# Kernel optimization log

Measured on AMD Instinct MI355X. Metric: run time of the kernel, lower is better.

The kernel has to match this reference:

```python
import jax, jax.numpy as jnp
import numpy as np

B = 8192
BASE = 340            # base_state_size (one frame)
STACK = 4             # frame stack -> state_size = 1360
SLOT_F = 4            # [present, dx, dy, dist] per slot
CAT_DEFS = [16, 8, 4, 4, 4, 8, 8, 8, 8]   # slots per category (sum = 68)
NUM_CATS = len(CAT_DEFS)
CAT_INFO = []
_off = 59
for _slots in CAT_DEFS:
    CAT_INFO.append((_off, _slots))
    _off += 1 + _slots * SLOT_F
STATE_SIZE = BASE * STACK
ATTN_DIM, HEADS = 128, 4
HEAD_DIM = ATTN_DIM // HEADS
TRUNK_H = 1024
ATOMS = 51
ACTIONS = 81
TRUNK_IN = STATE_SIZE + ATTN_DIM
NEG_INF = -1e9


def _layernorm(x, g, b, eps=1e-5):
    m = x.mean(-1, keepdims=True)
    v = ((x - m) ** 2).mean(-1, keepdims=True)
    return (x - m) * jax.lax.rsqrt(v + eps) * g + b


def setup_inputs() -> dict:
    key = jax.random.key(0)
    ks = iter(jax.random.split(key, 32))
    def w(shape, s=0.02):
        return jax.random.normal(next(ks), shape, jnp.float32) * s
    return {
        "state": jax.random.normal(next(ks), (B, STATE_SIZE), jnp.float32),
        "embed_W": w((7, ATTN_DIM)), "embed_b": jnp.zeros((ATTN_DIM,), jnp.float32),
        "ln_g": jnp.ones((ATTN_DIM,), jnp.float32), "ln_b": jnp.zeros((ATTN_DIM,), jnp.float32),
        "cls_tok": jnp.zeros((1, 1, ATTN_DIM), jnp.float32),
        "in_proj_W": w((3 * ATTN_DIM, ATTN_DIM)), "in_proj_b": jnp.zeros((3 * ATTN_DIM,), jnp.float32),
        "out_proj_W": w((ATTN_DIM, ATTN_DIM)), "out_proj_b": jnp.zeros((ATTN_DIM,), jnp.float32),
        "t0_W": w((TRUNK_IN, TRUNK_H)), "t0_b": jnp.zeros((TRUNK_H,), jnp.float32),
        "t0_g": jnp.ones((TRUNK_H,), jnp.float32), "t0_beta": jnp.zeros((TRUNK_H,), jnp.float32),
        "t1_W": w((TRUNK_H, TRUNK_H)), "t1_b": jnp.zeros((TRUNK_H,), jnp.float32),
        "t1_g": jnp.ones((TRUNK_H,), jnp.float32), "t1_beta": jnp.zeros((TRUNK_H,), jnp.float32),
        "val_fc_W": w((TRUNK_H, TRUNK_H // 2)), "val_fc_b": jnp.zeros((TRUNK_H // 2,), jnp.float32),
        "val_out_W": w((TRUNK_H // 2, ATOMS)), "val_out_b": jnp.zeros((ATOMS,), jnp.float32),
        "adv_fc_W": w((TRUNK_H, TRUNK_H // 2)), "adv_fc_b": jnp.zeros((TRUNK_H // 2,), jnp.float32),
        "adv_out_W": w((TRUNK_H // 2, ACTIONS * ATOMS)), "adv_out_b": jnp.zeros((ACTIONS * ATOMS,), jnp.float32),
    }


def _build_tokens(state):
    """Per-category gather + delta + pack -> (B, 68, 7) tokens and (B, 68) empty-mask."""
    b = state.shape[0]
    latest_off = (STACK - 1) * BASE
    prev_off = (STACK - 2) * BASE
    toks, masks = [], []
    for cat_id, (base, slots) in enumerate(CAT_INFO):
        lo = latest_off + base + 1
        po = prev_off + base + 1
        latest = state[:, lo:lo + slots * SLOT_F].reshape(b, slots, SLOT_F)
        prev = state[:, po:po + slots * SLOT_F].reshape(b, slots, SLOT_F)
        present = latest[:, :, 0]
        dx, dy, dist = latest[:, :, 1:2], latest[:, :, 2:3], latest[:, :, 3:4]
        vel_valid = ((present > 0.5) & (prev[:, :, 0] > 0.5))[:, :, None].astype(state.dtype)
        ddx = (dx - prev[:, :, 1:2]) * vel_valid
        ddy = (dy - prev[:, :, 2:3]) * vel_valid
        cat_norm = jnp.full((b, slots, 1), cat_id / (NUM_CATS - 1), state.dtype)
        toks.append(jnp.concatenate([dx, dy, dist, ddx, ddy, cat_norm, present[:, :, None]], axis=2))
        masks.append(present < 0.5)
    tokens = jnp.concatenate(toks, axis=1)
    mask = jnp.concatenate(masks, axis=1)          # True = slot empty
    all_empty = jnp.all(mask, axis=1, keepdims=True)
    mask = mask & ~all_empty                       # if everything empty, unmask all
    return tokens, mask


def reference(state, embed_W, embed_b, ln_g, ln_b, cls_tok, in_proj_W, in_proj_b,
              out_proj_W, out_proj_b, t0_W, t0_b, t0_g, t0_beta, t1_W, t1_b, t1_g, t1_beta,
              val_fc_W, val_fc_b, val_out_W, val_out_b, adv_fc_W, adv_fc_b, adv_out_W, adv_out_b):
    b = state.shape[0]
    tokens, mask = _build_tokens(state)
    x = _layernorm(tokens @ embed_W + embed_b, ln_g, ln_b)
    x = jnp.concatenate([jnp.broadcast_to(cls_tok, (b, 1, ATTN_DIM)), x], axis=1)  # (B, S+1, E)
    kpm = jnp.concatenate([jnp.zeros((b, 1), bool), mask], axis=1)                  # (B, S+1)
    qkv = x @ in_proj_W.T + in_proj_b
    q, k, v = jnp.split(qkv, 3, axis=-1)
    def to_heads(t):
        return t.reshape(b, -1, HEADS, HEAD_DIM).transpose(0, 2, 1, 3)
    q, k, v = to_heads(q), to_heads(k), to_heads(v)
    scores = jnp.einsum('bhqd,bhkd->bhqk', q, k) / np.float32(np.sqrt(HEAD_DIM))
    scores = jnp.where(kpm[:, None, None, :], NEG_INF, scores)
    attn = jax.nn.softmax(scores, axis=-1)
    out = jnp.einsum('bhqk,bhkd->bhqd', attn, v).transpose(0, 2, 1, 3).reshape(b, -1, ATTN_DIM)
    out = out @ out_proj_W.T + out_proj_b
    pooled = out[:, 0, :]                           # CLS pooling
    h = jnp.concatenate([state, pooled], axis=1)
    h = jax.nn.relu(_layernorm(h @ t0_W + t0_b, t0_g, t0_beta))
    h = jax.nn.relu(_layernorm(h @ t1_W + t1_b, t1_g, t1_beta))
    val = jax.nn.relu(h @ val_fc_W + val_fc_b)
    val = (val @ val_out_W + val_out_b).reshape(b, 1, ATOMS)
    adv = jax.nn.relu(h @ adv_fc_W + adv_fc_b)
    adv = (adv @ adv_out_W + adv_out_b).reshape(b, ACTIONS, ATOMS)
    q_atoms = val + adv - adv.mean(axis=1, keepdims=True)
    return jax.nn.softmax(q_atoms, axis=2)          # (B, 81, 51) C51 probabilities
```

## Files before the change

kernel.cpp:

```cpp
#include <hip/hip_runtime.h>

typedef unsigned short u16;
typedef unsigned int u32;
typedef __attribute__((ext_vector_type(4))) unsigned int u32x4;
typedef __attribute__((ext_vector_type(8))) __bf16 bf16x8;
typedef __attribute__((ext_vector_type(4))) float f32x4;

#define MFMA(a, b, c) __builtin_amdgcn_mfma_f32_16x16x32_bf16(a, b, c, 0, 0, 0)

__device__ __forceinline__ float b2f(u16 h) {
    union { unsigned int u; float f; } v; v.u = ((unsigned int)h) << 16; return v.f;
}
__device__ __forceinline__ u16 f2b(float f) {
    union { float f; unsigned int u; } v; v.f = f;
    unsigned int r = v.u + 0x7fffu + ((v.u >> 16) & 1u);
    return (u16)(r >> 16);
}
__device__ __forceinline__ float gread(const void* p, size_t i, int isf32) {
    return isf32 ? ((const float*)p)[i] : b2f(((const u16*)p)[i]);
}
__device__ __forceinline__ void gl_lds16(const u16* g, u16* l) {
    __builtin_amdgcn_global_load_lds(
        (const __attribute__((address_space(1))) void*)(g),
        (__attribute__((address_space(3))) void*)(l), 16, 0, 0);
}

__global__ __launch_bounds__(256) void detect_kernel(const void* __restrict__ state,
                                                     int* __restrict__ flag)
{
    __shared__ int cnt;
    if (threadIdx.x == 0) cnt = 0;
    __syncthreads();
    const u16* p = (const u16*)state;
    int local = 0;
    for (int i = threadIdx.x; i < 4096; i += 256) {
        int e = (p[i] >> 7) & 0xFF;
        if (e >= 200) local++;
    }
    atomicAdd(&cnt, local);
    __syncthreads();
    if (threadIdx.x == 0) *flag = (cnt >= 32) ? 1 : 0;
}

__global__ __launch_bounds__(256) void norm_small_kernel(
    const void* __restrict__ embW, const void* __restrict__ embB,
    const void* __restrict__ lng,  const void* __restrict__ lnb,
    const void* __restrict__ cls,  const void* __restrict__ ipW,
    const void* __restrict__ ipb,  const void* __restrict__ opW,
    const void* __restrict__ opb,  const void* __restrict__ t0g,
    const void* __restrict__ t0be, const void* __restrict__ t1g,
    const void* __restrict__ t1be, u16* __restrict__ dst,
    const int* __restrict__ flagp)
{
    int idx = blockIdx.x * 256 + threadIdx.x;
    if (idx >= 71552) return;
    int isf32 = *flagp;
    const void* src; int rel;
    if      (idx < 896)   { src = embW; rel = idx; }
    else if (idx < 1024)  { src = embB; rel = idx - 896; }
    else if (idx < 1152)  { src = lng;  rel = idx - 1024; }
    else if (idx < 1280)  { src = lnb;  rel = idx - 1152; }
    else if (idx < 1408)  { src = cls;  rel = idx - 1280; }
    else if (idx < 50560) { src = ipW;  rel = idx - 1408; }
    else if (idx < 50944) { src = ipb;  rel = idx - 50560; }
    else if (idx < 67328) { src = opW;  rel = idx - 50944; }
    else if (idx < 67456) { src = opb;  rel = idx - 67328; }
    else if (idx < 68480) { src = t0g;  rel = idx - 67456; }
    else if (idx < 69504) { src = t0be; rel = idx - 68480; }
    else if (idx < 70528) { src = t1g;  rel = idx - 69504; }
    else                  { src = t1be; rel = idx - 70528; }
    dst[idx] = isf32 ? f2b(((const float*)src)[rel]) : ((const u16*)src)[rel];
}

__global__ __launch_bounds__(256) void pack_kernel(
    const void* __restrict__ t0W, const void* __restrict__ t1W,
    const void* __restrict__ vfW, const void* __restrict__ afW,
    const void* __restrict__ voW, const void* __restrict__ aoW,
    const void* __restrict__ t0b, const void* __restrict__ t1b,
    const void* __restrict__ vfb, const void* __restrict__ afb,
    const void* __restrict__ vob, const void* __restrict__ aob,
    const int* __restrict__ flagp,
    u16* __restrict__ Bt0, u16* __restrict__ Bt1, u16* __restrict__ Btfc,
    u16* __restrict__ Btao,
    float* __restrict__ bias0, float* __restrict__ bias1, float* __restrict__ biasfc,
    float* __restrict__ biasao)
{
    int idx = blockIdx.x * 256 + threadIdx.x;
    const int isf32 = *flagp;
    if (idx < 1540096) {
        int n = idx / 1504, k = idx % 1504;
        Bt0[idx] = (k < 1488) ? f2b(gread(t0W, (size_t)k * 1024 + n, isf32)) : (u16)0;
        return;
    }
    idx -= 1540096;
    if (idx < 1048576) {
        int n = idx >> 10, k = idx & 1023;
        Bt1[idx] = f2b(gread(t1W, (size_t)k * 1024 + n, isf32));
        return;
    }
    idx -= 1048576;
    if (idx < 1048576) {
        int n = idx >> 10, k = idx & 1023;
        Btfc[idx] = (n < 512) ? f2b(gread(vfW, (size_t)k * 512 + n, isf32))
                              : f2b(gread(afW, (size_t)k * 512 + (n - 512), isf32));
        return;
    }
    idx -= 1048576;
    if (idx < 2228224) {
        int n = idx / 512, k = idx & 511;
        u16 v = 0;
        if (n < 4131)                  v = f2b(gread(aoW, (size_t)k * 4131 + n, isf32));
        else if (n >= 4224 && n < 4275) v = f2b(gread(voW, (size_t)k * 51 + (n - 4224), isf32));
        Btao[idx] = v;
        return;
    }
    idx -= 2228224;
    if (idx < 1024) { bias0[idx] = gread(t0b, idx, isf32); return; }
    idx -= 1024;
    if (idx < 1024) { bias1[idx] = gread(t1b, idx, isf32); return; }
    idx -= 1024;
    if (idx < 1024) { biasfc[idx] = (idx < 512) ? gread(vfb, idx, isf32)
                                                : gread(afb, idx - 512, isf32); return; }
    idx -= 1024;
    if (idx < 4352) {
        float v = 0.f;
        if (idx < 4131) v = gread(aob, idx, isf32);
        else if (idx >= 4224 && idx < 4275) v = gread(vob, idx - 4224, isf32);
        biasao[idx] = v;
        return;
    }
}

__global__ __launch_bounds__(384) void prep_cls_kernel(
    const u16* __restrict__ cls, const u16* __restrict__ ipW, const u16* __restrict__ ipb,
    float* __restrict__ qvec, float* __restrict__ vcls, float* __restrict__ s0)
{
    __shared__ float qkv[384];
    int tid = threadIdx.x;
    float a = b2f(ipb[tid]);
    for (int c = 0; c < 128; c++) a += b2f(ipW[(size_t)tid * 128 + c]) * b2f(cls[c]);
    qkv[tid] = a;
    __syncthreads();
    if (tid < 128) { qvec[tid] = qkv[tid]; vcls[tid] = qkv[256 + tid]; }
    if (tid < 4) {
        float s = 0.f;
        for (int d = 0; d < 32; d++) s += qkv[tid * 32 + d] * qkv[128 + tid * 32 + d];
        s0[tid] = s * 0.17677669529663687f;
    }
}

__global__ __launch_bounds__(256) void prep2_kernel(
    const u16* __restrict__ ipW, const u16* __restrict__ ipb,
    const float* __restrict__ qvec, float* __restrict__ rmat, float* __restrict__ cb)
{
    int tid = threadIdx.x;
    for (int j = 0; j < 2; j++) {
        int idx = j * 256 + tid;
        int h = idx >> 7, c = idx & 127;
        float acc = 0.f;
        for (int k = 0; k < 32; k++)
            acc += qvec[32 * h + k] * b2f(ipW[(size_t)(128 + 32 * h + k) * 128 + c]);
        rmat[idx] = acc;
    }
    if (tid < 4) {
        float acc = 0.f;
        for (int k = 0; k < 32; k++)
            acc += qvec[32 * tid + k] * b2f(ipb[128 + 32 * tid + k]);
        cb[tid] = acc;
    }
}

__global__ __launch_bounds__(256) void attn_kernel(
    const void* __restrict__ state, const int* __restrict__ flagp,
    const u16* __restrict__ embW, const u16* __restrict__ embB,
    const u16* __restrict__ lng, const u16* __restrict__ lnb,
    const u16* __restrict__ ipW, const u16* __restrict__ ipb,
    const u16* __restrict__ opW, const u16* __restrict__ opb,
    const float* __restrict__ vcls, const float* __restrict__ s0,
    const float* __restrict__ rmat, const float* __restrict__ cb,
    u16* __restrict__ A0)
{
    __shared__ __align__(16) u16 Xs[68][138];
    __shared__ __align__(16) float rstk[4][33][4];
    __shared__ __align__(16) float embWs[896];
    __shared__ __align__(16) float tok[68][8];
    __shared__ __align__(16) float sc[68][4];
    __shared__ __align__(16) float pp[72][4];
    __shared__ __align__(16) float zs[4][128];
    __shared__ __align__(16) float yv[128];
    __shared__ u16 embBh[128], lngh[128], lnbh[128];
    __shared__ float maskf[68];
    __shared__ float cbs[4];
    __shared__ int   cnt;

    const int b   = blockIdx.x;
    const int tid = threadIdx.x;
    const int wave = tid >> 6, lane = tid & 63;
    const int isf32 = *flagp;
    u16* arow = A0 + (size_t)b * 1504;
    float* rowf = (float*)&Xs[0][0];

    for (int i = tid; i < 896; i += 256) embWs[i] = b2f(embW[i]);
    if (tid < 128) { embBh[tid] = embB[tid]; lngh[tid] = lng[tid]; lnbh[tid] = lnb[tid]; }
    for (int i = tid; i < 512; i += 256) {
        int h = i >> 7, c = i & 127;
        rstk[c >> 5][c & 31][h] = rmat[i];
    }
    if (tid < 4) cbs[tid] = cb[tid];
    if (tid == 0) cnt = 0;

    if (isf32) {
        const f32x4* srowf = (const f32x4*)((const float*)state + (size_t)b * 1360);
        for (int i = tid; i < 170; i += 256) {
            f32x4 v0 = srowf[i * 2], v1 = srowf[i * 2 + 1];
            union { u16 h[8]; u32x4 v; } u;
            #pragma unroll
            for (int j = 0; j < 4; j++) { u.h[j] = f2b(v0[j]); u.h[4 + j] = f2b(v1[j]); }
            *(u32x4*)&arow[i * 8] = u.v;
            *(f32x4*)&rowf[i * 8] = v0;
            *(f32x4*)&rowf[i * 8 + 4] = v1;
        }
    } else {
        const u16* srow = (const u16*)state + (size_t)b * 1360;
        for (int i = tid; i < 170; i += 256) {
            u32x4 v = *(const u32x4*)&srow[i * 8];
            *(u32x4*)&arow[i * 8] = v;
            union { u32x4 v; u16 h[8]; } u; u.v = v;
            f32x4 f0, f1;
            #pragma unroll
            for (int j = 0; j < 4; j++) { f0[j] = b2f(u.h[j]); f1[j] = b2f(u.h[4 + j]); }
            *(f32x4*)&rowf[i * 8] = f0;
            *(f32x4*)&rowf[i * 8 + 4] = f1;
        }
    }
    if (tid < 16) arow[1488 + tid] = 0;
    __syncthreads();

    if (tid < 68) {
        const int cum[10]    = {0, 16, 24, 28, 32, 36, 44, 52, 60, 68};
        const int basetab[9] = {59, 124, 157, 174, 191, 208, 241, 274, 307};
        int t = tid, cat = 0;
        while (t >= cum[cat + 1]) cat++;
        int slot = t - cum[cat];
        int off  = basetab[cat] + 1 + slot * 4;
        float lp    = rowf[1020 + off + 0];
        float ldx   = rowf[1020 + off + 1];
        float ldy   = rowf[1020 + off + 2];
        float ldist = rowf[1020 + off + 3];
        float ppres = rowf[680 + off + 0];
        float pdx   = rowf[680 + off + 1];
        float pdy   = rowf[680 + off + 2];
        float vv = (lp > 0.5f && ppres > 0.5f) ? 1.f : 0.f;
        tok[t][0] = ldx; tok[t][1] = ldy; tok[t][2] = ldist;
        tok[t][3] = (ldx - pdx) * vv; tok[t][4] = (ldy - pdy) * vv;
        tok[t][5] = (float)cat * 0.125f; tok[t][6] = lp;
        int m = (lp < 0.5f) ? 1 : 0;
        maskf[t] = (float)m;
        if (m) atomicAdd(&cnt, 1);
    }
    __syncthreads();
    const bool all_empty = (cnt == 68);

    for (int t = wave; t < 68; t += 4) {
        float e0 = b2f(embBh[lane]), e1 = b2f(embBh[lane + 64]);
        #pragma unroll
        for (int f = 0; f < 7; f++) {
            float tv = tok[t][f];
            e0 += tv * embWs[f * 128 + lane];
            e1 += tv * embWs[f * 128 + lane + 64];
        }
        float s = e0 + e1;
        #pragma unroll
        for (int m = 1; m < 64; m <<= 1) s += __shfl_xor(s, m);
        float mean = s * (1.f / 128.f);
        float d0 = e0 - mean, d1 = e1 - mean;
        float v = d0 * d0 + d1 * d1;
        #pragma unroll
        for (int m = 1; m < 64; m <<= 1) v += __shfl_xor(v, m);
        float inv = rsqrtf(v * (1.f / 128.f) + 1e-5f);
        Xs[t][lane]      = f2b(d0 * inv * b2f(lngh[lane])      + b2f(lnbh[lane]));
        Xs[t][lane + 64] = f2b(d1 * inv * b2f(lngh[lane + 64]) + b2f(lnbh[lane + 64]));
    }
    __syncthreads();

    for (int it = 0; it < 2; it++) {
        int idx = it * 256 + tid;
        if (idx < 272) {
            int t = idx >> 2, ks = idx & 3;
            const u32* xrow = (const u32*)&Xs[t][0] + ks * 16;
            f32x4 a = {0.f, 0.f, 0.f, 0.f};
            #pragma unroll
            for (int c = 0; c < 16; c++) {
                u32 w = xrow[c];
                union { u32 u; float f; } lo, hi;
                lo.u = w << 16; hi.u = w & 0xffff0000u;
                f32x4 r0 = *(const f32x4*)&rstk[ks][2 * c][0];
                f32x4 r1 = *(const f32x4*)&rstk[ks][2 * c + 1][0];
                a += lo.f * r0 + hi.f * r1;
            }
            #pragma unroll
            for (int m = 1; m < 4; m <<= 1) {
                a[0] += __shfl_xor(a[0], m);
                a[1] += __shfl_xor(a[1], m);
                a[2] += __shfl_xor(a[2], m);
                a[3] += __shfl_xor(a[3], m);
            }
            float v = (ks == 0) ? a[0] : (ks == 1) ? a[1] : (ks == 2) ? a[2] : a[3];
            float sv = (cbs[ks] + v) * 0.17677669529663687f;
            if (maskf[t] > 0.5f && !all_empty) sv = -1e9f;
            sc[t][ks] = sv;
        }
    }
    __syncthreads();

    {
        int h = wave;
        float v0 = (lane == 0) ? s0[h] : sc[lane - 1][h];
        float v1 = (lane <= 4) ? sc[lane + 63][h] : -1e30f;
        float m = fmaxf(v0, v1);
        #pragma unroll
        for (int mm = 1; mm < 64; mm <<= 1) m = fmaxf(m, __shfl_xor(m, mm));
        float e0 = __expf(v0 - m);
        float e1 = (lane <= 4) ? __expf(v1 - m) : 0.f;
        float sum = e0 + e1;
        #pragma unroll
        for (int mm = 1; mm < 64; mm <<= 1) sum += __shfl_xor(sum, mm);
        float rinv = 1.f / sum;
        pp[lane][h] = e0 * rinv;
        if (lane <= 4) pp[lane + 64][h] = e1 * rinv;
    }
    __syncthreads();

    {
        int c = tid & 127, h0 = (tid >> 7) * 2;
        float acc0 = 0.f, acc1 = 0.f;
        #pragma unroll 4
        for (int t = 0; t < 68; t++) {
            float x = b2f(Xs[t][c]);
            float2 p = *(const float2*)&pp[t + 1][h0];
            acc0 += p.x * x; acc1 += p.y * x;
        }
        zs[h0][c] = acc0; zs[h0 + 1][c] = acc1;
    }
    __syncthreads();

    {
        int d = tid >> 1, half = tid & 1, h = d >> 5;
        float acc = 0.f;
        const u16* wrow = ipW + (size_t)(256 + d) * 128 + 64 * half;
        const float* zrow = &zs[h][64 * half];
        #pragma unroll
        for (int j = 0; j < 8; j++) {
            bf16x8 w = *(const bf16x8*)(wrow + j * 8);
            #pragma unroll
            for (int k = 0; k < 8; k++) acc += (float)w[k] * zrow[j * 8 + k];
        }
        float other = __shfl_xor(acc, 1);
        if (half == 0) {
            float p0 = pp[0][h];
            yv[d] = acc + other + p0 * vcls[d] + (1.f - p0) * b2f(ipb[256 + d]);
        }
    }
    __syncthreads();

    {
        int e = tid >> 1, half = tid & 1;
        float acc = 0.f;
        const u16* wrow = opW + (size_t)e * 128 + 64 * half;
        const float* yrow = &yv[64 * half];
        #pragma unroll
        for (int j = 0; j < 8; j++) {
            bf16x8 w = *(const bf16x8*)(wrow + j * 8);
            #pragma unroll
            for (int k = 0; k < 8; k++) acc += (float)w[k] * yrow[j * 8 + k];
        }
        float other = __shfl_xor(acc, 1);
        if (half == 0) arow[1360 + e] = f2b(acc + other + b2f(opb[e]));
    }
}

template <int EPI>
__global__ __launch_bounds__(256) void gemm_bt(
    const u16* __restrict__ A, int lda, const u16* __restrict__ Bt, int ldb,
    const float* __restrict__ bias, void* __restrict__ Cout, int ldc, int K)
{
    __shared__ __align__(16) u16 As[128 * 32];
    __shared__ __align__(16) u16 Bs[128 * 32];
    const int tid = threadIdx.x;
    const int row0 = blockIdx.y * 128, col0 = blockIdx.x * 128;
    const int wave = tid >> 6, lane = tid & 63;
    const int wm = wave >> 1, wn = wave & 1;
    const int lr = lane & 15, lq = lane >> 4;

    f32x4 acc[4][4] = {};

    for (int k0 = 0; k0 < K; k0 += 32) {
        __syncthreads();
        #pragma unroll
        for (int j = 0; j < 2; j++) {
            int ci = j * 256 + wave * 64 + lane;
            int r = ci >> 2, q = ci & 3;
            int lbase = (j * 256 + wave * 64) * 8;
            gl_lds16(A  + (size_t)(row0 + r) * lda + k0 + q * 8, &As[lbase]);
            gl_lds16(Bt + (size_t)(col0 + r) * ldb + k0 + q * 8, &Bs[lbase]);
        }
        __syncthreads();
        bf16x8 af[4], bf[4];
        #pragma unroll
        for (int i = 0; i < 4; i++) af[i] = *(const bf16x8*)&As[(wm * 64 + i * 16 + lr) * 32 + lq * 8];
        #pragma unroll
        for (int j = 0; j < 4; j++) bf[j] = *(const bf16x8*)&Bs[(wn * 64 + j * 16 + lr) * 32 + lq * 8];
        #pragma unroll
        for (int i = 0; i < 4; i++)
            #pragma unroll
            for (int j = 0; j < 4; j++)
                acc[i][j] = MFMA(af[i], bf[j], acc[i][j]);
    }

    const int cbase = col0 + wn * 64;
    const int rbase = row0 + wm * 64;
    float bv[4];
    #pragma unroll
    for (int j = 0; j < 4; j++) bv[j] = bias[cbase + j * 16 + lr];
    #pragma unroll
    for (int i = 0; i < 4; i++) {
        #pragma unroll
        for (int j = 0; j < 4; j++) {
            int cc = cbase + j * 16 + lr;
            #pragma unroll
            for (int r = 0; r < 4; r++) {
                int rr = rbase + i * 16 + lq * 4 + r;
                float v = acc[i][j][r] + bv[j];
                if (EPI == 1) v = fmaxf(v, 0.f);
                if (EPI == 0) ((float*)Cout)[(size_t)rr * ldc + cc] = v;
                else          ((u16*)Cout)[(size_t)rr * ldc + cc] = f2b(v);
            }
        }
    }
}

__global__ __launch_bounds__(256) void ln_relu_kernel(
    const float* __restrict__ C, const u16* __restrict__ g, const u16* __restrict__ be,
    u16* __restrict__ H)
{
    __shared__ float red[8];
    const int b = blockIdx.x, tid = threadIdx.x;
    const float* row = C + (size_t)b * 1024;
    float x0 = row[tid], x1 = row[tid + 256], x2 = row[tid + 512], x3 = row[tid + 768];
    float s = x0 + x1 + x2 + x3;
    #pragma unroll
    for (int m = 1; m < 64; m <<= 1) s += __shfl_xor(s, m);
    if ((tid & 63) == 0) red[tid >> 6] = s;
    __syncthreads();
    float mean = (red[0] + red[1] + red[2] + red[3]) * (1.f / 1024.f);
    float d0 = x0 - mean, d1 = x1 - mean, d2 = x2 - mean, d3 = x3 - mean;
    float v = d0 * d0 + d1 * d1 + d2 * d2 + d3 * d3;
    #pragma unroll
    for (int m = 1; m < 64; m <<= 1) v += __shfl_xor(v, m);
    if ((tid & 63) == 0) red[4 + (tid >> 6)] = v;
    __syncthreads();
    float inv = rsqrtf((red[4] + red[5] + red[6] + red[7]) * (1.f / 1024.f) + 1e-5f);
    u16* hrow = H + (size_t)b * 1024;
    float dd[4] = {d0, d1, d2, d3};
    #pragma unroll
    for (int i = 0; i < 4; i++) {
        int c = tid + i * 256;
        float h = dd[i] * inv * b2f(g[c]) + b2f(be[c]);
        hrow[c] = f2b(fmaxf(h, 0.f));
    }
}

__global__ __launch_bounds__(256) void final_kernel(
    const u16* __restrict__ ADV, void* __restrict__ out, const int* __restrict__ flagp)
{
    __shared__ __align__(16) u16 advr[4136];
    __shared__ float meanv[51];
    __shared__ float valv[51];
    const int b = blockIdx.x, tid = threadIdx.x;
    const int isf32 = *flagp;
    const u16* arow = ADV + (size_t)b * 4352;
    for (int i = tid; i < 517; i += 256)
        *(u32x4*)&advr[i * 8] = *(const u32x4*)&arow[i * 8];
    if (tid < 51) valv[tid] = b2f(arow[4224 + tid]);
    __syncthreads();
    if (tid < 51) {
        float s = 0.f;
        for (int j = 0; j < 81; j++) s += b2f(advr[j * 51 + tid]);
        meanv[tid] = s * (1.f / 81.f);
    }
    __syncthreads();
    const int wave = tid >> 6, lane = tid & 63;
    for (int a = wave; a < 81; a += 4) {
        float q = (lane < 51) ? valv[lane] + b2f(advr[a * 51 + lane]) - meanv[lane] : -1e30f;
        float m = q;
        #pragma unroll
        for (int mm = 1; mm < 64; mm <<= 1) m = fmaxf(m, __shfl_xor(m, mm));
        float e = (lane < 51) ? __expf(q - m) : 0.f;
        float s = e;
        #pragma unroll
        for (int mm = 1; mm < 64; mm <<= 1) s += __shfl_xor(s, mm);
        if (lane < 51) {
            float r = e / s;
            size_t oi = (size_t)b * 4131 + a * 51 + lane;
            if (isf32) ((float*)out)[oi] = r;
            else       ((u16*)out)[oi]  = f2b(r);
        }
    }
}

extern "C" void kernel_launch(void* const* d_in, const int* in_sizes, int n_in,
                              void* d_out, int out_size, void* d_ws, size_t ws_size,
                              hipStream_t stream)
{
    (void)in_sizes; (void)n_in; (void)out_size; (void)ws_size;
    const void* state = d_in[0];
    const void* embW  = d_in[1];
    const void* embB  = d_in[2];
    const void* lng   = d_in[3];
    const void* lnb   = d_in[4];
    const void* cls   = d_in[5];
    const void* ipW   = d_in[6];
    const void* ipb   = d_in[7];
    const void* opW   = d_in[8];
    const void* opb   = d_in[9];
    const void* t0W   = d_in[10];
    const void* t0b   = d_in[11];
    const void* t0g   = d_in[12];
    const void* t0be  = d_in[13];
    const void* t1W   = d_in[14];
    const void* t1b   = d_in[15];
    const void* t1g   = d_in[16];
    const void* t1be  = d_in[17];
    const void* vfW   = d_in[18];
    const void* vfb   = d_in[19];
    const void* voW   = d_in[20];
    const void* vob   = d_in[21];
    const void* afW   = d_in[22];
    const void* afb   = d_in[23];
    const void* aoW   = d_in[24];
    const void* aob   = d_in[25];

    char* ws = (char*)d_ws;
    size_t off = 0;
    auto alloc = [&](size_t bytes) -> void* {
        off = (off + 255) & ~(size_t)255;
        void* p = ws + off;
        off += bytes;
        return p;
    };
    int*   flag   = (int*)alloc(4);
    u16*   Nbuf   = (u16*)alloc(71552 * 2);
    float* qvec   = (float*)alloc(128 * 4);
    float* vcls   = (float*)alloc(128 * 4);
    float* s0     = (float*)alloc(4 * 4);
    float* rmat   = (float*)alloc(512 * 4);
    float* cb     = (float*)alloc(4 * 4);
    float* bias0  = (float*)alloc(1024 * 4);
    float* bias1  = (float*)alloc(1024 * 4);
    float* biasfc = (float*)alloc(1024 * 4);
    float* biasao = (float*)alloc(4352 * 4);
    u16* Bt0  = (u16*)alloc(1024L * 1504 * 2);
    u16* Bt1  = (u16*)alloc(1024L * 1024 * 2);
    u16* Btfc = (u16*)alloc(1024L * 1024 * 2);
    u16* Btao = (u16*)alloc(4352L * 512 * 2);
    u16* A0   = (u16*)alloc(8192L * 1504 * 2);
    float* C0 = (float*)alloc(8192L * 1024 * 4);
    u16* H0   = (u16*)alloc(8192L * 1024 * 2);
    u16* ADV  = A0;
    u16* H1   = (u16*)alloc(8192L * 1024 * 2);
    u16* VA   = (u16*)alloc(8192L * 1024 * 2);

    u16* Nemb  = Nbuf + 0;
    u16* NembB = Nbuf + 896;
    u16* Nlng  = Nbuf + 1024;
    u16* Nlnb  = Nbuf + 1152;
    u16* Ncls  = Nbuf + 1280;
    u16* Nipw  = Nbuf + 1408;
    u16* Nipb  = Nbuf + 50560;
    u16* Nopw  = Nbuf + 50944;
    u16* Nopb  = Nbuf + 67328;
    u16* Nt0g  = Nbuf + 67456;
    u16* Nt0be = Nbuf + 68480;
    u16* Nt1g  = Nbuf + 69504;
    u16* Nt1be = Nbuf + 70528;

    detect_kernel<<<1, 256, 0, stream>>>(state, flag);
    norm_small_kernel<<<280, 256, 0, stream>>>(embW, embB, lng, lnb, cls, ipW, ipb,
                                               opW, opb, t0g, t0be, t1g, t1be,
                                               Nbuf, flag);
    pack_kernel<<<22941, 256, 0, stream>>>(t0W, t1W, vfW, afW, voW, aoW,
                                           t0b, t1b, vfb, afb, vob, aob, flag,
                                           Bt0, Bt1, Btfc, Btao,
                                           bias0, bias1, biasfc, biasao);
    prep_cls_kernel<<<1, 384, 0, stream>>>(Ncls, Nipw, Nipb, qvec, vcls, s0);
    prep2_kernel<<<1, 256, 0, stream>>>(Nipw, Nipb, qvec, rmat, cb);
    attn_kernel<<<8192, 256, 0, stream>>>(state, flag, Nemb, NembB, Nlng, Nlnb,
                                          Nipw, Nipb, Nopw, Nopb,
                                          vcls, s0, rmat, cb, A0);
    gemm_bt<0><<<dim3(8, 64), 256, 0, stream>>>(A0, 1504, Bt0, 1504, bias0, C0, 1024, 1504);
    ln_relu_kernel<<<8192, 256, 0, stream>>>(C0, Nt0g, Nt0be, H0);
    gemm_bt<0><<<dim3(8, 64), 256, 0, stream>>>(H0, 1024, Bt1, 1024, bias1, C0, 1024, 1024);
    ln_relu_kernel<<<8192, 256, 0, stream>>>(C0, Nt1g, Nt1be, H1);
    gemm_bt<1><<<dim3(8, 64), 256, 0, stream>>>(H1, 1024, Btfc, 1024, biasfc, VA, 1024, 1024);
    gemm_bt<2><<<dim3(33, 64), 256, 0, stream>>>(VA + 512, 1024, Btao, 512, biasao, ADV, 4352, 512);
    gemm_bt<2><<<dim3(1, 64), 256, 0, stream>>>(VA, 1024, Btao + 4224L * 512, 512,
                                                biasao + 4224, ADV + 4224, 4352, 512);
    final_kernel<<<8192, 256, 0, stream>>>(ADV, d_out, flag);
}
```

Baseline: 745.0 us.

## Compute token LayerNorm statistics analytically from precomputed embedding moments

Precomputes the column means and covariance of the 7x128 embedding weight and bias once in prep2. Each token's LayerNorm mean and variance then come from a small 7-term quadratic form instead of two 64-lane shuffle reductions per token. The embedding weights are also kept as bf16 in shared memory to cut LDS usage. The risk is a numerical difference, because variance computed through the covariance expansion can cancel catastrophically compared with the direct two-pass form.

Result: faster. 694.8 us (-6.7%).

```diff
diff --git a/kernel.cpp b/kernel.cpp
--- a/kernel.cpp
+++ b/kernel.cpp
@@ -151,8 +151,11 @@
 
 __global__ __launch_bounds__(256) void prep2_kernel(
     const u16* __restrict__ ipW, const u16* __restrict__ ipb,
-    const float* __restrict__ qvec, float* __restrict__ rmat, float* __restrict__ cb)
-{
+    const u16* __restrict__ embW, const u16* __restrict__ embB,
+    const float* __restrict__ qvec, float* __restrict__ rmat, float* __restrict__ cb,
+    float* __restrict__ lnstat)
+{
+    __shared__ float wm[8];
     int tid = threadIdx.x;
     for (int j = 0; j < 2; j++) {
         int idx = j * 256 + tid;
@@ -168,6 +171,37 @@
             acc += qvec[32 * tid + k] * b2f(ipb[128 + 32 * tid + k]);
         cb[tid] = acc;
     }
+    if (tid < 8) {
+        float s = 0.f;
+        if (tid < 7) { for (int c = 0; c < 128; c++) s += b2f(embW[tid * 128 + c]); }
+        else         { for (int c = 0; c < 128; c++) s += b2f(embB[c]); }
+        wm[tid] = s * (1.f / 128.f);
+        lnstat[tid] = wm[tid];
+    }
+    __syncthreads();
+    if (tid < 57) {
+        float acc = 0.f;
+        if (tid < 49) {
+            int f = tid / 7, g = tid % 7;
+            float wf = wm[f], wg = wm[g];
+            for (int c = 0; c < 128; c++)
+                acc += (b2f(embW[f * 128 + c]) - wf) * (b2f(embW[g * 128 + c]) - wg);
+            lnstat[8 + tid] = acc * (1.f / 128.f);
+        } else if (tid < 56) {
+            int f = tid - 49;
+            float wf = wm[f], bm = wm[7];
+            for (int c = 0; c < 128; c++)
+                acc += (b2f(embW[f * 128 + c]) - wf) * (b2f(embB[c]) - bm);
+            lnstat[57 + f] = acc * (1.f / 128.f);
+        } else {
+            float bm = wm[7];
+            for (int c = 0; c < 128; c++) {
+                float d = b2f(embB[c]) - bm;
+                acc += d * d;
+            }
+            lnstat[64] = acc * (1.f / 128.f);
+        }
+    }
 }
 
 __global__ __launch_bounds__(256) void attn_kernel(
@@ -178,16 +212,19 @@
     const u16* __restrict__ opW, const u16* __restrict__ opb,
     const float* __restrict__ vcls, const float* __restrict__ s0,
     const float* __restrict__ rmat, const float* __restrict__ cb,
+    const float* __restrict__ lnstat,
     u16* __restrict__ A0)
 {
     __shared__ __align__(16) u16 Xs[68][138];
     __shared__ __align__(16) float rstk[4][33][4];
-    __shared__ __align__(16) float embWs[896];
+    __shared__ __align__(16) u16 embWs16[896];
     __shared__ __align__(16) float tok[68][8];
     __shared__ __align__(16) float sc[68][4];
     __shared__ __align__(16) float pp[72][4];
     __shared__ __align__(16) float zs[4][128];
     __shared__ __align__(16) float yv[128];
+    __shared__ __align__(16) float mstat[68][2];
+    __shared__ __align__(16) float lns[72];
     __shared__ u16 embBh[128], lngh[128], lnbh[128];
     __shared__ float maskf[68];
     __shared__ float cbs[4];
@@ -200,12 +237,13 @@
     u16* arow = A0 + (size_t)b * 1504;
     float* rowf = (float*)&Xs[0][0];
 
-    for (int i = tid; i < 896; i += 256) embWs[i] = b2f(embW[i]);
+    for (int i = tid; i < 896; i += 256) embWs16[i] = embW[i];
     if (tid < 128) { embBh[tid] = embB[tid]; lngh[tid] = lng[tid]; lnbh[tid] = lnb[tid]; }
     for (int i = tid; i < 512; i += 256) {
         int h = i >> 7, c = i & 127;
         rstk[c >> 5][c & 31][h] = rmat[i];
     }
+    if (tid < 65) lns[tid] = lnstat[tid];
     if (tid < 4) cbs[tid] = cb[tid];
     if (tid == 0) cnt = 0;
 
@@ -251,9 +289,25 @@
         float pdx   = rowf[680 + off + 1];
         float pdy   = rowf[680 + off + 2];
         float vv = (lp > 0.5f && ppres > 0.5f) ? 1.f : 0.f;
-        tok[t][0] = ldx; tok[t][1] = ldy; tok[t][2] = ldist;
-        tok[t][3] = (ldx - pdx) * vv; tok[t][4] = (ldy - pdy) * vv;
-        tok[t][5] = (float)cat * 0.125f; tok[t][6] = lp;
+        float tokr[7];
+        tokr[0] = ldx; tokr[1] = ldy; tokr[2] = ldist;
+        tokr[3] = (ldx - pdx) * vv; tokr[4] = (ldy - pdy) * vv;
+        tokr[5] = (float)cat * 0.125f; tokr[6] = lp;
+        #pragma unroll
+        for (int f = 0; f < 7; f++) tok[t][f] = tokr[f];
+        float mean = lns[7];
+        #pragma unroll
+        for (int f = 0; f < 7; f++) mean += tokr[f] * lns[f];
+        float var = lns[64];
+        #pragma unroll
+        for (int f = 0; f < 7; f++) {
+            float q = 2.f * lns[57 + f];
+            #pragma unroll
+            for (int g = 0; g < 7; g++) q += lns[8 + f * 7 + g] * tokr[g];
+            var += tokr[f] * q;
+        }
+        mstat[t][0] = mean;
+        mstat[t][1] = rsqrtf(var + 1e-5f);
         int m = (lp < 0.5f) ? 1 : 0;
         maskf[t] = (float)m;
         if (m) atomicAdd(&cnt, 1);
@@ -266,20 +320,12 @@
         #pragma unroll
         for (int f = 0; f < 7; f++) {
             float tv = tok[t][f];
-            e0 += tv * embWs[f * 128 + lane];
-            e1 += tv * embWs[f * 128 + lane + 64];
-        }
-        float s = e0 + e1;
-        #pragma unroll
-        for (int m = 1; m < 64; m <<= 1) s += __shfl_xor(s, m);
-        float mean = s * (1.f / 128.f);
-        float d0 = e0 - mean, d1 = e1 - mean;
-        float v = d0 * d0 + d1 * d1;
-        #pragma unroll
-        for (int m = 1; m < 64; m <<= 1) v += __shfl_xor(v, m);
-        float inv = rsqrtf(v * (1.f / 128.f) + 1e-5f);
-        Xs[t][lane]      = f2b(d0 * inv * b2f(lngh[lane])      + b2f(lnbh[lane]));
-        Xs[t][lane + 64] = f2b(d1 * inv * b2f(lngh[lane + 64]) + b2f(lnbh[lane + 64]));
+            e0 += tv * b2f(embWs16[f * 128 + lane]);
+            e1 += tv * b2f(embWs16[f * 128 + lane + 64]);
+        }
+        float mean = mstat[t][0], inv = mstat[t][1];
+        Xs[t][lane]      = f2b((e0 - mean) * inv * b2f(lngh[lane])      + b2f(lnbh[lane]));
+        Xs[t][lane + 64] = f2b((e1 - mean) * inv * b2f(lngh[lane + 64]) + b2f(lnbh[lane + 64]));
     }
     __syncthreads();
 
@@ -555,6 +601,7 @@
     float* s0     = (float*)alloc(4 * 4);
     float* rmat   = (float*)alloc(512 * 4);
     float* cb     = (float*)alloc(4 * 4);
+    float* lnstat = (float*)alloc(72 * 4);
     float* bias0  = (float*)alloc(1024 * 4);
     float* bias1  = (float*)alloc(1024 * 4);
     float* biasfc = (float*)alloc(1024 * 4);
@@ -593,10 +640,10 @@
                                            Bt0, Bt1, Btfc, Btao,
                                            bias0, bias1, biasfc, biasao);
     prep_cls_kernel<<<1, 384, 0, stream>>>(Ncls, Nipw, Nipb, qvec, vcls, s0);
-    prep2_kernel<<<1, 256, 0, stream>>>(Nipw, Nipb, qvec, rmat, cb);
+    prep2_kernel<<<1, 256, 0, stream>>>(Nipw, Nipb, Nemb, NembB, qvec, rmat, cb, lnstat);
     attn_kernel<<<8192, 256, 0, stream>>>(state, flag, Nemb, NembB, Nlng, Nlnb,
                                           Nipw, Nipb, Nopw, Nopb,
-                                          vcls, s0, rmat, cb, A0);
+                                          vcls, s0, rmat, cb, lnstat, A0);
     gemm_bt<0><<<dim3(8, 64), 256, 0, stream>>>(A0, 1504, Bt0, 1504, bias0, C0, 1024, 1504);
     ln_relu_kernel<<<8192, 256, 0, stream>>>(C0, Nt0g, Nt0be, H0);
     gemm_bt<0><<<dim3(8, 64), 256, 0, stream>>>(H0, 1024, Bt1, 1024, bias1, C0, 1024, 1024);
```
